# Kernel optimization log

Measured on AMD Instinct MI355X. Metric: run time of the kernel, lower is better.

## Reference

```python
import jax, jax.numpy as jnp
import numpy as np

INPUT_DIM = 1024
NUM_TARGETS = 128
BATCH = 32768


def setup_inputs() -> dict:
    key = jax.random.key(0)
    kx, kw, kb = jax.random.split(key, 3)
    x = jax.random.normal(kx, (BATCH, INPUT_DIM), dtype=jnp.float32)
    # Fused view of num_targets independent nn.Linear(input_dim, 1) layers:
    # column t of W / entry t of b are the weights/bias of layer t.
    bound = 1.0 / np.sqrt(INPUT_DIM)  # torch Linear default init range
    W = jax.random.uniform(kw, (INPUT_DIM, NUM_TARGETS), minval=-bound, maxval=bound, dtype=jnp.float32)
    b = jax.random.uniform(kb, (NUM_TARGETS,), minval=-bound, maxval=bound, dtype=jnp.float32)
    return {"x": x, "W": W, "b": b}


def reference(x, W, b):
    # Equivalent to concatenating sigmoid(Linear_t(x)) over t along last dim:
    # one fused matmul [B,D]x[D,T] + bias + sigmoid.
    return jax.nn.sigmoid(x @ W + b)
```

## Files before the change

### kernel.cpp

```cpp
#include <hip/hip_runtime.h>
#include <hip/hip_bf16.h>


typedef __bf16 bf16x8 __attribute__((ext_vector_type(8)));
typedef float  f32x4  __attribute__((ext_vector_type(4)));

#define DIM   1024
#define NT    128
#define BATCH 32768

__global__ __launch_bounds__(256) void prep_w(const float* __restrict__ W,
                                              __bf16* __restrict__ wsW) {
    int idx = blockIdx.x * 256 + threadIdx.x;
    int j = idx & 7;
    int l = (idx >> 3) & 63;
    int c = (idx >> 9) & 7;
    int s = idx >> 12;
    int k = s * 32 + (l >> 4) * 8 + j;
    int n = c * 16 + (l & 15);
    wsW[idx] = (__bf16)W[k * NT + n];
}

__device__ __forceinline__ bf16x8 cvt_bf16x8(float4 a0, float4 a1) {
    bf16x8 af;
    af[0] = (__bf16)a0.x; af[1] = (__bf16)a0.y;
    af[2] = (__bf16)a0.z; af[3] = (__bf16)a0.w;
    af[4] = (__bf16)a1.x; af[5] = (__bf16)a1.y;
    af[6] = (__bf16)a1.z; af[7] = (__bf16)a1.w;
    return af;
}

__global__ __launch_bounds__(256) void gemm_bias_sigmoid(
        const float* __restrict__ x,
        const __hip_bfloat16* __restrict__ wsWh,
        const float* __restrict__ bias,
        float* __restrict__ out) {
    const __bf16* wsW = (const __bf16*)wsWh;
    const int lane = threadIdx.x & 63;
    const int wave = threadIdx.x >> 6;
    const int q    = lane >> 4;
    const int r    = lane & 15;
    const int row0 = blockIdx.x * 64 + wave * 16;

    const float* xA = x + (size_t)(row0 + r) * DIM + q * 8;
    const bf16x8* wb = (const bf16x8*)wsW + lane;

    f32x4 acc[8];
#pragma unroll
    for (int c = 0; c < 8; ++c)
        acc[c] = (f32x4){0.f, 0.f, 0.f, 0.f};

    float4 aA0, aA1, aB0, aB1;
    bf16x8 bA[8], bB[8];

    aA0 = *(const float4*)(xA);
    aA1 = *(const float4*)(xA + 4);
#pragma unroll
    for (int c = 0; c < 8; ++c)
        bA[c] = wb[(size_t)c * 64];

    for (int t = 0; t < 16; ++t) {
        const int s1 = 2 * t + 1;
        const int s2 = 2 * t + 2;

        {
            const float* ap = xA + (size_t)s1 * 32;
            aB0 = *(const float4*)ap;
            aB1 = *(const float4*)(ap + 4);
            const bf16x8* wp = wb + (size_t)s1 * 512;
#pragma unroll
            for (int c = 0; c < 8; ++c)
                bB[c] = wp[(size_t)c * 64];
        }

        {
            const bf16x8 af = cvt_bf16x8(aA0, aA1);
#pragma unroll
            for (int c = 0; c < 8; ++c)
                acc[c] = __builtin_amdgcn_mfma_f32_16x16x32_bf16(af, bA[c], acc[c], 0, 0, 0);
        }

        if (t < 15) {
            const float* ap = xA + (size_t)s2 * 32;
            aA0 = *(const float4*)ap;
            aA1 = *(const float4*)(ap + 4);
            const bf16x8* wp = wb + (size_t)s2 * 512;
#pragma unroll
            for (int c = 0; c < 8; ++c)
                bA[c] = wp[(size_t)c * 64];
        }

        {
            const bf16x8 af = cvt_bf16x8(aB0, aB1);
#pragma unroll
            for (int c = 0; c < 8; ++c)
                acc[c] = __builtin_amdgcn_mfma_f32_16x16x32_bf16(af, bB[c], acc[c], 0, 0, 0);
        }
    }

#pragma unroll
    for (int c = 0; c < 8; ++c) {
        const float bv = bias[c * 16 + r];
#pragma unroll
        for (int reg = 0; reg < 4; ++reg) {
            const int row = row0 + q * 4 + reg;
            float v = acc[c][reg] + bv;
            v = 1.0f / (1.0f + __expf(-v));
            out[(size_t)row * NT + c * 16 + r] = v;
        }
    }
}

extern "C" void kernel_launch(void* const* d_in, const int* in_sizes, int n_in,
                              void* d_out, int out_size, void* d_ws, size_t ws_size,
                              hipStream_t stream) {
    const float* x = (const float*)d_in[0];
    const float* W = (const float*)d_in[1];
    const float* b = (const float*)d_in[2];
    float* out     = (float*)d_out;
    __bf16* wsW    = (__bf16*)d_ws;

    prep_w<<<DIM * NT / 256, 256, 0, stream>>>(W, wsW);
    gemm_bias_sigmoid<<<BATCH / 64, 256, 0, stream>>>(
        x, (const __hip_bfloat16*)wsW, b, out);
}
```

Measured before the change: 215.2 us.

## Stage bf16 weights through shared LDS and batch x prefetch per phase

Loads the pre-swizzled bf16 weight matrix into a 64 KB LDS buffer in four phases, shared by all four waves of the block, instead of each wave reading its fragments from global memory. x rows are prefetched four k-slices at a time into register arrays, double-buffered across the phase halves. This cuts duplicate L2 weight traffic per block and keeps more x loads in flight. It adds block barriers per phase, exposes the weight staging latency, and the large LDS footprint and register arrays lower occupancy.

```diff
diff --git a/kernel.cpp b/kernel.cpp
--- a/kernel.cpp
+++ b/kernel.cpp
@@ -35,66 +35,72 @@
         const __hip_bfloat16* __restrict__ wsWh,
         const float* __restrict__ bias,
         float* __restrict__ out) {
-    const __bf16* wsW = (const __bf16*)wsWh;
-    const int lane = threadIdx.x & 63;
-    const int wave = threadIdx.x >> 6;
+    const bf16x8* __restrict__ wsW8 = (const bf16x8*)wsWh;
+    __shared__ bf16x8 ldsW[4096];
+
+    const int tid  = threadIdx.x;
+    const int lane = tid & 63;
+    const int wave = tid >> 6;
     const int q    = lane >> 4;
     const int r    = lane & 15;
     const int row0 = blockIdx.x * 64 + wave * 16;
 
     const float* xA = x + (size_t)(row0 + r) * DIM + q * 8;
-    const bf16x8* wb = (const bf16x8*)wsW + lane;
 
     f32x4 acc[8];
 #pragma unroll
     for (int c = 0; c < 8; ++c)
         acc[c] = (f32x4){0.f, 0.f, 0.f, 0.f};
 
-    float4 aA0, aA1, aB0, aB1;
-    bf16x8 bA[8], bB[8];
+    float4 S0[8], S1[8];
 
-    aA0 = *(const float4*)(xA);
-    aA1 = *(const float4*)(xA + 4);
 #pragma unroll
-    for (int c = 0; c < 8; ++c)
-        bA[c] = wb[(size_t)c * 64];
+    for (int i = 0; i < 4; ++i) {
+        const float* ap = xA + (size_t)i * 32;
+        S0[2 * i]     = *(const float4*)ap;
+        S0[2 * i + 1] = *(const float4*)(ap + 4);
+    }
 
-    for (int t = 0; t < 16; ++t) {
-        const int s1 = 2 * t + 1;
-        const int s2 = 2 * t + 2;
+    for (int p = 0; p < 4; ++p) {
+        __syncthreads();
+#pragma unroll
+        for (int i = 0; i < 16; ++i) {
+            const int e = tid + i * 256;
+            ldsW[e] = wsW8[p * 4096 + e];
+        }
+#pragma unroll
+        for (int i = 0; i < 4; ++i) {
+            const float* ap = xA + (size_t)(p * 8 + 4 + i) * 32;
+            S1[2 * i]     = *(const float4*)ap;
+            S1[2 * i + 1] = *(const float4*)(ap + 4);
+        }
+        __syncthreads();
 
-        {
-            const float* ap = xA + (size_t)s1 * 32;
-            aB0 = *(const float4*)ap;
-            aB1 = *(const float4*)(ap + 4);
-            const bf16x8* wp = wb + (size_t)s1 * 512;
 #pragma unroll
-            for (int c = 0; c < 8; ++c)
-                bB[c] = wp[(size_t)c * 64];
+        for (int sl = 0; sl < 4; ++sl) {
+            const bf16x8 af = cvt_bf16x8(S0[2 * sl], S0[2 * sl + 1]);
+#pragma unroll
+            for (int c = 0; c < 8; ++c) {
+                const bf16x8 bf = ldsW[(sl * 8 + c) * 64 + lane];
+                acc[c] = __builtin_amdgcn_mfma_f32_16x16x32_bf16(af, bf, acc[c], 0, 0, 0);
+            }
         }
-
-        {
-            const bf16x8 af = cvt_bf16x8(aA0, aA1);
+        if (p < 3) {
 #pragma unroll
-            for (int c = 0; c < 8; ++c)
-                acc[c] = __builtin_amdgcn_mfma_f32_16x16x32_bf16(af, bA[c], acc[c], 0, 0, 0);
+            for (int i = 0; i < 4; ++i) {
+                const float* ap = xA + (size_t)((p + 1) * 8 + i) * 32;
+                S0[2 * i]     = *(const float4*)ap;
+                S0[2 * i + 1] = *(const float4*)(ap + 4);
+            }
         }
-
-        if (t < 15) {
-            const float* ap = xA + (size_t)s2 * 32;
-            aA0 = *(const float4*)ap;
-            aA1 = *(const float4*)(ap + 4);
-            const bf16x8* wp = wb + (size_t)s2 * 512;
 #pragma unroll
-            for (int c = 0; c < 8; ++c)
-                bA[c] = wp[(size_t)c * 64];
-        }
-
-        {
-            const bf16x8 af = cvt_bf16x8(aB0, aB1);
+        for (int sl = 4; sl < 8; ++sl) {
+            const bf16x8 af = cvt_bf16x8(S1[2 * (sl - 4)], S1[2 * (sl - 4) + 1]);
 #pragma unroll
-            for (int c = 0; c < 8; ++c)
-                acc[c] = __builtin_amdgcn_mfma_f32_16x16x32_bf16(af, bB[c], acc[c], 0, 0, 0);
+            for (int c = 0; c < 8; ++c) {
+                const bf16x8 bf = ldsW[(sl * 8 + c) * 64 + lane];
+                acc[c] = __builtin_amdgcn_mfma_f32_16x16x32_bf16(af, bf, acc[c], 0, 0, 0);
+            }
         }
     }
 
```

New measurement: 203.5 us. 5.5% less time.
